# Kernel tuning notes

Hardware: AMD Instinct MI355X
Metric: run time of the kernel (lower is better)

## Reference

```python
import jax, jax.numpy as jnp
import numpy as np

H = 512   # layer_size
D = 5     # dim
B = 64
T = 512
EPS = 1e-3  # Keras BatchNormalization default epsilon


def _p(key, shape, scale=0.05):
    return jax.random.normal(key, shape, dtype=jnp.float32) * scale


def setup_inputs() -> dict:
    key = jax.random.key(0)
    ks = jax.random.split(key, 32)
    inp = {
        "x": jax.random.normal(ks[0], (B, T, D), dtype=jnp.float32),
        # LSTM 1 (input D)
        "W1": _p(ks[1], (D, 4 * H)), "U1": _p(ks[2], (H, 4 * H)), "b1": jnp.zeros((4 * H,), jnp.float32),
        # BatchNorm on H features (inference: moving stats)
        "g1": jnp.ones((H,), jnp.float32), "be1": jnp.zeros((H,), jnp.float32),
        "m1": _p(ks[3], (H,), 0.1), "v1": jnp.ones((H,), jnp.float32) + jax.random.uniform(ks[4], (H,)) * 0.1,
        # LSTM 2 (input H)
        "W2": _p(ks[5], (H, 4 * H)), "U2": _p(ks[6], (H, 4 * H)), "b2": jnp.zeros((4 * H,), jnp.float32),
        # LSTM 3 (input H, returns last state only)
        "W3": _p(ks[7], (H, 4 * H)), "U3": _p(ks[8], (H, 4 * H)), "b3": jnp.zeros((4 * H,), jnp.float32),
        # dense head y
        "d1w": _p(ks[9], (H, 32)), "d1b": jnp.zeros((32,), jnp.float32),
        "g2": jnp.ones((32,), jnp.float32), "be2": jnp.zeros((32,), jnp.float32),
        "m2": _p(ks[10], (32,), 0.1), "v2": jnp.ones((32,), jnp.float32) + jax.random.uniform(ks[11], (32,)) * 0.1,
        "d2w": _p(ks[12], (32, 16)), "d2b": jnp.zeros((16,), jnp.float32),
        "hw": _p(ks[13], (16, 1)), "hb": jnp.zeros((1,), jnp.float32),
        # dense head z
        "d4w": _p(ks[14], (H, 128)), "d4b": jnp.zeros((128,), jnp.float32),
        "d5w": _p(ks[15], (128, 64)), "d5b": jnp.zeros((64,), jnp.float32),
        "rw": _p(ks[16], (64, D)), "rb": jnp.zeros((D,), jnp.float32),
    }
    return inp


def lstm(x, W, U, b):
    """Keras LSTM, gate order i,f,c,o. x: [B,T,din] -> (seq [B,T,H], h_T, c_T)."""
    xz = jnp.einsum('btd,dk->btk', x, W) + b  # precompute input projections [B,T,4H]

    def step(carry, xz_t):
        h, c = carry
        z = xz_t + h @ U
        i, f, g, o = jnp.split(z, 4, axis=-1)
        i = jax.nn.sigmoid(i)
        f = jax.nn.sigmoid(f)
        g = jnp.tanh(g)
        o = jax.nn.sigmoid(o)
        c = f * c + i * g
        h = o * jnp.tanh(c)
        return (h, c), h

    b_ = x.shape[0]
    h0 = jnp.zeros((b_, U.shape[0]), x.dtype)
    (hT, cT), hs = jax.lax.scan(step, (h0, h0), jnp.swapaxes(xz, 0, 1))
    return jnp.swapaxes(hs, 0, 1), hT, cT


def bn_inf(x, g, b, m, v):
    return (x - m) * (g / jnp.sqrt(v + EPS)) + b


def reference(x, W1, U1, b1, g1, be1, m1, v1, W2, U2, b2, W3, U3, b3,
              d1w, d1b, g2, be2, m2, v2, d2w, d2b, hw, hb,
              d4w, d4b, d5w, d5b, rw, rb):
    # inference: GaussianNoise / Dropout are identity
    x1, h1, s1 = lstm(x, W1, U1, b1)          # [B,T,H]
    xr = bn_inf(x1, g1, be1, m1, v1)
    x2, h2, s2 = lstm(xr, W2, U2, b2)         # [B,T,H]
    xs = x1 + x2                               # residual Add
    _, h3, s3 = lstm(xs, W3, U3, b3)           # last hidden state [B,H]
    xlast = h3
    # head y
    y = xlast @ d1w + d1b
    y = bn_inf(y, g2, be2, m2, v2)
    y = y @ d2w + d2b
    y = jax.nn.sigmoid(y @ hw + hb)            # [B,1]
    # head z
    z = xlast @ d4w + d4b
    z = z @ d5w + d5b
    z = z @ rw + rb                            # [B,D]
    return (y, z)
```

## Files before the change

kernel.cpp:

```cpp
#include <hip/hip_runtime.h>
#include <hip/hip_bf16.h>

typedef short bf16x8 __attribute__((ext_vector_type(8)));
typedef float f32x4 __attribute__((ext_vector_type(4)));
typedef unsigned short u16;
typedef unsigned int u32;
typedef unsigned long long u64;

#define EPSBN 1e-3f

__device__ __forceinline__ u16 f2b(float f){
  unsigned u = __float_as_uint(f);
  return (u16)((u + 0x7fffu + ((u >> 16) & 1u)) >> 16);
}
__device__ __forceinline__ float b2f(u16 v){ return __uint_as_float(((unsigned)v) << 16); }
__device__ __forceinline__ float sigm(float x){ return 1.f/(1.f + __expf(-x)); }
__device__ __forceinline__ float tanhx(float x){ return 2.f/(1.f + __expf(-2.f*x)) - 1.f; }

union U64x2 { u64 q[2]; bf16x8 v; };
union BP    { u32 p[4]; bf16x8 v; };


__global__ void prep_sv(const float* __restrict__ g1, const float* __restrict__ be1,
                        const float* __restrict__ m1, const float* __restrict__ v1,
                        float* __restrict__ s, float* __restrict__ tv){
  int k = blockIdx.x*256 + threadIdx.x;
  if (k < 512){
    float sv = g1[k] * rsqrtf(v1[k] + EPSBN);
    s[k] = sv;
    tv[k] = be1[k] - m1[k]*sv;
  }
}

__global__ void prep_b2p(const float* __restrict__ W2, const float* __restrict__ b2,
                         const float* __restrict__ tv, float* __restrict__ out){
  int col = blockIdx.x*256 + threadIdx.x;
  float acc = b2[col];
  for (int k=0;k<512;++k) acc += tv[k] * W2[(size_t)k*2048 + col];
  out[col] = acc;
}

__global__ void transpose_pack(const float* __restrict__ in, const float* __restrict__ scale,
                               u16* __restrict__ out){
  __shared__ float tile[64][65];
  int k0 = blockIdx.x * 64;
  int c0 = blockIdx.y * 64;
  int t = threadIdx.x;
  int cc = t & 63, kk0 = (t >> 6) * 16;
  #pragma unroll
  for (int i=0;i<16;++i){
    float v = in[(size_t)(k0 + kk0 + i)*2048 + c0 + cc];
    if (scale) v *= scale[k0 + kk0 + i];
    tile[kk0 + i][cc] = v;
  }
  __syncthreads();
  int cc2 = t >> 2, kp = t & 3;
  int col = c0 + cc2;
  int hcol = col & 511;
  int row = (hcol >> 5)*128 + (col >> 9)*32 + ((hcol >> 4) & 1)*16 + (col & 15);
  bf16x8 v0, v1;
  #pragma unroll
  for (int i=0;i<8;++i){
    v0[i] = (short)f2b(tile[kp*16 + i][cc2]);
    v1[i] = (short)f2b(tile[kp*16 + 8 + i][cc2]);
  }
  u16* dst = out + (size_t)row*512 + k0 + kp*16;
  *(bf16x8*)dst = v0;
  *(bf16x8*)(dst + 8) = v1;
}

__global__ void pack_w1(const float* __restrict__ W1, u16* __restrict__ out){
  int r = blockIdx.x*256 + threadIdx.x;
  int wg = r >> 7, q = (r >> 5) & 3, jt = (r >> 4) & 1, jj = r & 15;
  int col = q*512 + wg*32 + jt*16 + jj;
  #pragma unroll
  for (int k=0;k<32;++k)
    out[(size_t)r*32 + k] = (k < 5) ? f2b(W1[(size_t)k*2048 + col]) : (u16)0;
}

__global__ void pack_x(const float* __restrict__ x, u16* __restrict__ out){
  int i = blockIdx.x*256 + threadIdx.x;
  int k = i & 31;
  int bt = i >> 5;
  out[i] = (k < 5) ? f2b(x[(size_t)bt*5 + k]) : (u16)0;
}

__global__ void __launch_bounds__(256, 1) scan_all(
    const u16* __restrict__ Ure1, const u16* __restrict__ Ure2, const u16* __restrict__ Ure3,
    const u16* __restrict__ W1p,  const u16* __restrict__ W2p,  const u16* __restrict__ W3p,
    const u16* __restrict__ xpad,
    const float* __restrict__ b1, const float* __restrict__ b2p, const float* __restrict__ b3,
    u32* __restrict__ hbuf_all,
    u32* __restrict__ x1seq,
    u32* __restrict__ xsseq,
    float* __restrict__ h3out, u32* __restrict__ cnt)
{
  const int bid = blockIdx.x;
  const int phase = bid >> 6;
  const int b6 = bid & 63;
  const int g = b6 & 3, wg = b6 >> 2;
  const int tid = threadIdx.x;
  const int w = tid >> 6, l = tid & 63;
  const int lm = l & 15, lh = l >> 4;
  const int bg0 = g * 16;
  const int b_own = tid & 15, jl = tid >> 4;
  const int pb = tid >> 4, pj = tid & 15;

  const u16* Ure  = phase == 0 ? Ure1 : (phase == 1 ? Ure2 : Ure3);
  const u16* Wre  = phase == 0 ? W1p  : (phase == 1 ? W2p  : W3p);
  const float* bias = phase == 0 ? b1 : (phase == 1 ? b2p : b3);
  u32* hbuf32 = hbuf_all + (size_t)phase * 65536;
  u32* seqout = phase == 0 ? x1seq : (phase == 1 ? xsseq : nullptr);
  const u32* upseq = phase == 1 ? x1seq : (phase == 2 ? xsseq : nullptr);

  u32* cq  = cnt + (phase*4 + g)*64;
  const u32* upq = (phase > 0) ? cnt + ((phase-1)*4 + g)*64 : nullptr;

  bf16x8 aU[8][4];
  #pragma unroll
  for (int q=0;q<4;++q)
    #pragma unroll
    for (int jt=0;jt<2;++jt){
      const u16* up = Ure + (size_t)(wg*128 + q*32 + jt*16 + lm)*512 + w*128 + lh*8;
      #pragma unroll
      for (int ks=0;ks<4;++ks) aU[q*2+jt][ks] = *(const bf16x8*)(up + ks*32);
    }
  bf16x8 aW[8][4];
  if (phase == 0){
    #pragma unroll
    for (int q=0;q<4;++q)
      #pragma unroll
      for (int jt=0;jt<2;++jt)
        aW[q*2+jt][0] = *(const bf16x8*)(Wre + (size_t)(wg*128 + q*32 + jt*16 + lm)*32 + lh*8);
  } else {
    #pragma unroll
    for (int q=0;q<4;++q)
      #pragma unroll
      for (int jt=0;jt<2;++jt){
        const u16* wp = Wre + (size_t)(wg*128 + q*32 + jt*16 + lm)*512 + w*128 + lh*8;
        #pragma unroll
        for (int ks=0;ks<4;++ks) aW[q*2+jt][ks] = *(const bf16x8*)(wp + ks*32);
      }
  }

  float bias_g[4][2];
  #pragma unroll
  for (int q=0;q<4;++q){
    bias_g[q][0] = bias[q*512 + wg*32 + jl];
    bias_g[q][1] = bias[q*512 + wg*32 + jl + 16];
  }

  float cs0 = 0.f, cs1 = 0.f;

  __shared__ float zex[8][4][16][18];
  __shared__ u16 hsh[16][34];
  __shared__ u16 xsh[16][34];
  __shared__ u32 x1w[16][17];

  const u64 tagmask = 0x0000FFFF0000FFFFull;

  for (int t=0; t<512; ++t){
    f32x4 acc[8] = {};

    if (phase == 0){
      if (w == 0){
        bf16x8 bx = *(const bf16x8*)(xpad + ((size_t)(bg0+lm)*512 + t)*32 + lh*8);
        #pragma unroll
        for (int i=0;i<8;++i)
          acc[i] = __builtin_amdgcn_mfma_f32_16x16x32_bf16(aW[i][0], bx, acc[i], 0,0,0);
      }
    } else {
      if (tid == 0){
        const u32 target = (u32)(16*(t+1));
        while (__hip_atomic_load(upq, __ATOMIC_RELAXED, __HIP_MEMORY_SCOPE_AGENT) < target) {}
      }
      __syncthreads();
      if (phase == 1){
        u32 rv = __hip_atomic_load(upseq + ((size_t)(bg0+pb)*512 + t)*256 + wg*16 + pj,
                                   __ATOMIC_RELAXED, __HIP_MEMORY_SCOPE_AGENT);
        x1w[pb][pj] = rv;
      }
      const u64* xp = (const u64*)upseq + ((size_t)(bg0+lm)*512 + t)*128 + w*32 + lh*2;
      U64x2 xq[4];
      #pragma unroll
      for (int ks=0;ks<4;++ks){
        xq[ks].q[0] = __hip_atomic_load(xp + ks*8,     __ATOMIC_RELAXED, __HIP_MEMORY_SCOPE_AGENT);
        xq[ks].q[1] = __hip_atomic_load(xp + ks*8 + 1, __ATOMIC_RELAXED, __HIP_MEMORY_SCOPE_AGENT);
      }
      #pragma unroll
      for (int ks=0;ks<4;++ks){
        #pragma unroll
        for (int i=0;i<8;++i)
          acc[i] = __builtin_amdgcn_mfma_f32_16x16x32_bf16(aW[i][ks], xq[ks].v, acc[i], 0,0,0);
      }
    }

    if (t > 0){
      const int slot = (t+1) & 1;
      const u64* hp = (const u64*)hbuf32
                    + (size_t)(slot*64 + bg0 + lm)*256 + w*64 + lh*4;
      const u32 tg = (u32)t;
      const u64 want = (u64)tg | ((u64)tg << 32);
      u64 raw[16];
      bool ok;
      do {
        #pragma unroll
        for (int ks=0;ks<4;++ks)
          #pragma unroll
          for (int qq=0;qq<4;++qq)
            raw[ks*4+qq] = __hip_atomic_load(hp + ks*16 + qq,
                                             __ATOMIC_RELAXED, __HIP_MEMORY_SCOPE_AGENT);
        u64 bad = 0;
        #pragma unroll
        for (int i=0;i<16;++i) bad |= (raw[i] & tagmask) ^ want;
        ok = __all(bad == 0);
      } while (!ok);
      #pragma unroll
      for (int ks=0;ks<4;++ks){
        BP bp;
        #pragma unroll
        for (int qq=0;qq<4;++qq){
          u32 lo = (u32)raw[ks*4+qq];
          u32 hi = (u32)(raw[ks*4+qq] >> 32);
          bp.p[qq] = (lo >> 16) | (hi & 0xFFFF0000u);
        }
        #pragma unroll
        for (int i=0;i<8;++i)
          acc[i] = __builtin_amdgcn_mfma_f32_16x16x32_bf16(aU[i][ks], bp.v, acc[i], 0,0,0);
      }
    }

    #pragma unroll
    for (int i=0;i<8;++i){
      #pragma unroll
      for (int r=0;r<4;++r)
        zex[i][w][lh*4 + r][lm] = acc[i][r];
    }
    __syncthreads();

    float hv0, hv1;
    {
      float zv[4][2];
      #pragma unroll
      for (int q=0;q<4;++q){
        #pragma unroll
        for (int s2=0;s2<2;++s2)
          zv[q][s2] = zex[q*2+s2][0][jl][b_own] + zex[q*2+s2][1][jl][b_own]
                    + zex[q*2+s2][2][jl][b_own] + zex[q*2+s2][3][jl][b_own] + bias_g[q][s2];
      }
      float iv = sigm(zv[0][0]), fv = sigm(zv[1][0]), gv = tanhx(zv[2][0]), ov = sigm(zv[3][0]);
      cs0 = fv * cs0 + iv * gv;
      hv0 = ov * tanhx(cs0);
      iv = sigm(zv[0][1]); fv = sigm(zv[1][1]); gv = tanhx(zv[2][1]); ov = sigm(zv[3][1]);
      cs1 = fv * cs1 + iv * gv;
      hv1 = ov * tanhx(cs1);
    }

    hsh[b_own][jl]      = f2b(hv0);
    hsh[b_own][jl + 16] = f2b(hv1);
    if (phase == 1){
      u32 w0 = x1w[b_own][jl >> 1], w1 = x1w[b_own][8 + (jl >> 1)];
      float x1r0 = b2f((u16)((jl & 1) ? (w0 >> 16) : (w0 & 0xffffu)));
      float x1r1 = b2f((u16)((jl & 1) ? (w1 >> 16) : (w1 & 0xffffu)));
      xsh[b_own][jl]      = f2b(x1r0 + hv0);
      xsh[b_own][jl + 16] = f2b(x1r1 + hv1);
    }
    if (phase == 2 && t == 511){
      h3out[(size_t)(bg0+b_own)*512 + wg*32 + jl]      = hv0;
      h3out[(size_t)(bg0+b_own)*512 + wg*32 + jl + 16] = hv1;
    }
    __syncthreads();

    {
      const int pslot = t & 1;
      const u32 tagv = (u32)(t + 1);
      u32 w0 = ((u32)hsh[pb][2*pj]     << 16) | tagv;
      u32 w1 = ((u32)hsh[pb][2*pj + 1] << 16) | tagv;
      __hip_atomic_store((u64*)(hbuf32 + (size_t)(pslot*64 + bg0 + pb)*512 + wg*32) + pj,
                         (u64)w0 | ((u64)w1 << 32),
                         __ATOMIC_RELAXED, __HIP_MEMORY_SCOPE_AGENT);
    }

    if (phase < 2){
      u32 sv;
      if (phase == 0) sv = (u32)hsh[pb][2*pj] | ((u32)hsh[pb][2*pj+1] << 16);
      else            sv = (u32)xsh[pb][2*pj] | ((u32)xsh[pb][2*pj+1] << 16);
      __hip_atomic_store(seqout + ((size_t)(bg0+pb)*512 + t)*256 + wg*16 + pj, sv,
                         __ATOMIC_RELAXED, __HIP_MEMORY_SCOPE_AGENT);
      asm volatile("s_waitcnt vmcnt(0)" ::: "memory");
      __syncthreads();
      if (tid == 0)
        __hip_atomic_fetch_add(cq, 1u, __ATOMIC_RELAXED, __HIP_MEMORY_SCOPE_AGENT);
    }
  }
}

__global__ void __launch_bounds__(256) head_k(
    const float* __restrict__ h3,
    const float* __restrict__ d1w, const float* __restrict__ d1b,
    const float* __restrict__ g2, const float* __restrict__ be2,
    const float* __restrict__ m2, const float* __restrict__ v2,
    const float* __restrict__ d2w, const float* __restrict__ d2b,
    const float* __restrict__ hw, const float* __restrict__ hb,
    const float* __restrict__ d4w, const float* __restrict__ d4b,
    const float* __restrict__ d5w, const float* __restrict__ d5b,
    const float* __restrict__ rw, const float* __restrict__ rb,
    float* __restrict__ out)
{
  __shared__ float hl[512];
  __shared__ float a1[32], a2[16], c1[128], c2[64];
  int b = blockIdx.x, t = threadIdx.x;
  for (int i=t; i<512; i+=256) hl[i] = h3[(size_t)b*512 + i];
  __syncthreads();
  if (t < 32){
    float acc = d1b[t];
    for (int k=0;k<512;++k) acc += hl[k] * d1w[(size_t)k*32 + t];
    a1[t] = (acc - m2[t]) * (g2[t] * rsqrtf(v2[t] + EPSBN)) + be2[t];
  } else if (t >= 128){
    int i = t - 128;
    float acc = d4b[i];
    for (int k=0;k<512;++k) acc += hl[k] * d4w[(size_t)k*128 + i];
    c1[i] = acc;
  }
  __syncthreads();
  if (t < 16){
    float acc = d2b[t];
    for (int k=0;k<32;++k) acc += a1[k] * d2w[k*16 + t];
    a2[t] = acc;
  } else if (t >= 64 && t < 128){
    int i = t - 64;
    float acc = d5b[i];
    for (int k=0;k<128;++k) acc += c1[k] * d5w[k*64 + i];
    c2[i] = acc;
  }
  __syncthreads();
  if (t == 0){
    float acc = hb[0];
    for (int k=0;k<16;++k) acc += a2[k] * hw[k];
    out[b] = 1.f/(1.f + __expf(-acc));
  } else if (t >= 32 && t < 37){
    int i = t - 32;
    float acc = rb[i];
    for (int k=0;k<64;++k) acc += c2[k] * rw[k*5 + i];
    out[64 + b*5 + i] = acc;
  }
}

extern "C" void kernel_launch(void* const* d_in, const int* in_sizes, int n_in,
                              void* d_out, int out_size, void* d_ws, size_t ws_size,
                              hipStream_t stream)
{
  const float* x   = (const float*)d_in[0];
  const float* W1  = (const float*)d_in[1];
  const float* U1  = (const float*)d_in[2];
  const float* b1  = (const float*)d_in[3];
  const float* g1  = (const float*)d_in[4];
  const float* be1 = (const float*)d_in[5];
  const float* m1  = (const float*)d_in[6];
  const float* v1  = (const float*)d_in[7];
  const float* W2  = (const float*)d_in[8];
  const float* U2  = (const float*)d_in[9];
  const float* b2  = (const float*)d_in[10];
  const float* W3  = (const float*)d_in[11];
  const float* U3  = (const float*)d_in[12];
  const float* b3  = (const float*)d_in[13];
  const float* d1w = (const float*)d_in[14];
  const float* d1b = (const float*)d_in[15];
  const float* g2  = (const float*)d_in[16];
  const float* be2 = (const float*)d_in[17];
  const float* m2  = (const float*)d_in[18];
  const float* v2  = (const float*)d_in[19];
  const float* d2w = (const float*)d_in[20];
  const float* d2b = (const float*)d_in[21];
  const float* hw  = (const float*)d_in[22];
  const float* hb  = (const float*)d_in[23];
  const float* d4w = (const float*)d_in[24];
  const float* d4b = (const float*)d_in[25];
  const float* d5w = (const float*)d_in[26];
  const float* d5b = (const float*)d_in[27];
  const float* rw  = (const float*)d_in[28];
  const float* rb  = (const float*)d_in[29];

  char* ws = (char*)d_ws;
  constexpr size_t SZ_W   = 2048ull*512*2;
  constexpr size_t o_Ure1 = 0;
  constexpr size_t o_Ure2 = o_Ure1 + SZ_W;
  constexpr size_t o_Ure3 = o_Ure2 + SZ_W;
  constexpr size_t o_W2p  = o_Ure3 + SZ_W;
  constexpr size_t o_W3p  = o_W2p + SZ_W;
  constexpr size_t o_W1p  = o_W3p + SZ_W;
  constexpr size_t o_xpad = o_W1p + 2048ull*32*2;
  constexpr size_t o_b2p  = o_xpad + 64ull*512*32*2;
  constexpr size_t o_s    = o_b2p + 2048ull*4;
  constexpr size_t o_tv   = o_s + 512ull*4;
  constexpr size_t o_h3   = o_tv + 512ull*4;
  constexpr size_t o_h    = o_h3 + 64ull*512*4;
  constexpr size_t SZ_HP  = 2ull*64*512*4;
  constexpr size_t SZ_H   = 3*SZ_HP;
  constexpr size_t o_cnt  = o_h + SZ_H;
  constexpr size_t o_x1   = o_cnt + 4096;
  constexpr size_t o_xs   = o_x1 + 64ull*512*512*2;

  u16* Ure1 = (u16*)(ws + o_Ure1);
  u16* Ure2 = (u16*)(ws + o_Ure2);
  u16* Ure3 = (u16*)(ws + o_Ure3);
  u16* W2p  = (u16*)(ws + o_W2p);
  u16* W3p  = (u16*)(ws + o_W3p);
  u16* W1p  = (u16*)(ws + o_W1p);
  u16* xpad = (u16*)(ws + o_xpad);
  u32* x1p  = (u32*)(ws + o_x1);
  u32* xsp  = (u32*)(ws + o_xs);

  hipMemsetAsync(ws + o_h, 0, SZ_H + 4096, stream);

  prep_sv<<<dim3(2), dim3(256), 0, stream>>>(g1, be1, m1, v1, (float*)(ws+o_s), (float*)(ws+o_tv));
  transpose_pack<<<dim3(8,32), dim3(256), 0, stream>>>(U1, nullptr, Ure1);
  transpose_pack<<<dim3(8,32), dim3(256), 0, stream>>>(U2, nullptr, Ure2);
  transpose_pack<<<dim3(8,32), dim3(256), 0, stream>>>(U3, nullptr, Ure3);
  transpose_pack<<<dim3(8,32), dim3(256), 0, stream>>>(W3, nullptr, W3p);
  transpose_pack<<<dim3(8,32), dim3(256), 0, stream>>>(W2, (const float*)(ws+o_s), W2p);
  prep_b2p<<<dim3(8), dim3(256), 0, stream>>>(W2, b2, (const float*)(ws+o_tv), (float*)(ws+o_b2p));
  pack_w1<<<dim3(8), dim3(256), 0, stream>>>(W1, W1p);
  pack_x<<<dim3(4096), dim3(256), 0, stream>>>(x, xpad);

  scan_all<<<dim3(192), dim3(256), 0, stream>>>(
      Ure1, Ure2, Ure3, W1p, W2p, W3p, xpad,
      b1, (const float*)(ws+o_b2p), b3,
      (u32*)(ws+o_h), x1p, xsp,
      (float*)(ws+o_h3), (u32*)(ws+o_cnt));

  head_k<<<dim3(64), dim3(256), 0, stream>>>((const float*)(ws+o_h3),
      d1w, d1b, g2, be2, m2, v2, d2w, d2b, hw, hb, d4w, d4b, d5w, d5b, rw, rb,
      (float*)d_out);
}
```

Before: 2.892 ms.

## Prefetch next-step upstream inputs and remove shared-memory staging in LSTM scan

Each thread now owns a pair of adjacent hidden units per batch row, so the gate results go straight to the global h-buffer and sequence output without passing through hsh/xsh/x1w shared arrays. The third __syncthreads is dropped and a raw s_barrier is used. The upstream-layer activations and x for step t+1 are prefetched during step t, with a non-blocking poll on the producer counter. The counter increment is deferred to the next step's barrier, which removes the per-step vmcnt(0) drain. The cost is a looser memory ordering: the counter publish relies on the barrier and implicit ordering of the earlier stores rather than an explicit wait, which could expose stale reads.

```diff
diff --git a/kernel.cpp b/kernel.cpp
--- a/kernel.cpp
+++ b/kernel.cpp
@@ -83,6 +83,10 @@
   int k = i & 31;
   int bt = i >> 5;
   out[i] = (k < 5) ? f2b(x[(size_t)bt*5 + k]) : (u16)0;
+}
+
+__device__ __forceinline__ void pollge(const u32* p, u32 target){
+  while (__hip_atomic_load(p, __ATOMIC_RELAXED, __HIP_MEMORY_SCOPE_AGENT) < target) {}
 }
 
 __global__ void __launch_bounds__(256, 1) scan_all(
@@ -103,8 +107,8 @@
   const int w = tid >> 6, l = tid & 63;
   const int lm = l & 15, lh = l >> 4;
   const int bg0 = g * 16;
-  const int b_own = tid & 15, jl = tid >> 4;
-  const int pb = tid >> 4, pj = tid & 15;
+  const int jp = tid & 15, gb = tid >> 4;
+  const int ti0 = jp >> 3;
 
   const u16* Ure  = phase == 0 ? Ure1 : (phase == 1 ? Ure2 : Ure3);
   const u16* Wre  = phase == 0 ? W1p  : (phase == 1 ? W2p  : W3p);
@@ -126,12 +130,15 @@
       for (int ks=0;ks<4;++ks) aU[q*2+jt][ks] = *(const bf16x8*)(up + ks*32);
     }
   bf16x8 aW[8][4];
+  bf16x8 aW1[8];
   if (phase == 0){
-    #pragma unroll
-    for (int q=0;q<4;++q)
-      #pragma unroll
-      for (int jt=0;jt<2;++jt)
-        aW[q*2+jt][0] = *(const bf16x8*)(Wre + (size_t)(wg*128 + q*32 + jt*16 + lm)*32 + lh*8);
+    if (w == 0){
+      #pragma unroll
+      for (int q=0;q<4;++q)
+        #pragma unroll
+        for (int jt=0;jt<2;++jt)
+          aW1[q*2+jt] = *(const bf16x8*)(Wre + (size_t)(wg*128 + q*32 + jt*16 + lm)*32 + lh*8);
+    }
   } else {
     #pragma unroll
     for (int q=0;q<4;++q)
@@ -143,50 +150,52 @@
       }
   }
 
-  float bias_g[4][2];
+  float bias0[4], bias1[4];
   #pragma unroll
   for (int q=0;q<4;++q){
-    bias_g[q][0] = bias[q*512 + wg*32 + jl];
-    bias_g[q][1] = bias[q*512 + wg*32 + jl + 16];
+    bias0[q] = bias[q*512 + wg*32 + 2*jp];
+    bias1[q] = bias[q*512 + wg*32 + 2*jp + 1];
   }
 
   float cs0 = 0.f, cs1 = 0.f;
 
   __shared__ float zex[8][4][16][18];
-  __shared__ u16 hsh[16][34];
-  __shared__ u16 xsh[16][34];
-  __shared__ u32 x1w[16][17];
-
   const u64 tagmask = 0x0000FFFF0000FFFFull;
+
+  U64x2 xq[4];
+  bf16x8 bx;
+  u32 rv = 0;
+  if (phase == 0){
+    if (w == 0)
+      bx = *(const bf16x8*)(xpad + ((size_t)(bg0+lm)*512 + 0)*32 + lh*8);
+  } else {
+    pollge(upq, 16u);
+    const u64* xp = (const u64*)upseq + ((size_t)(bg0+lm)*512 + 0)*128 + w*32 + lh*2;
+    #pragma unroll
+    for (int ks=0;ks<4;++ks){
+      xq[ks].q[0] = __hip_atomic_load(xp + ks*8,     __ATOMIC_RELAXED, __HIP_MEMORY_SCOPE_AGENT);
+      xq[ks].q[1] = __hip_atomic_load(xp + ks*8 + 1, __ATOMIC_RELAXED, __HIP_MEMORY_SCOPE_AGENT);
+    }
+    if (phase == 1)
+      rv = __hip_atomic_load(upseq + ((size_t)(bg0+gb)*512 + 0)*256 + wg*16 + jp,
+                             __ATOMIC_RELAXED, __HIP_MEMORY_SCOPE_AGENT);
+  }
 
   for (int t=0; t<512; ++t){
     f32x4 acc[8] = {};
+    const u32 rvc = rv;
+
+    u32 upv = 0xffffffffu;
+    if (phase > 0 && t < 511)
+      upv = __hip_atomic_load(upq, __ATOMIC_RELAXED, __HIP_MEMORY_SCOPE_AGENT);
 
     if (phase == 0){
       if (w == 0){
-        bf16x8 bx = *(const bf16x8*)(xpad + ((size_t)(bg0+lm)*512 + t)*32 + lh*8);
         #pragma unroll
         for (int i=0;i<8;++i)
-          acc[i] = __builtin_amdgcn_mfma_f32_16x16x32_bf16(aW[i][0], bx, acc[i], 0,0,0);
+          acc[i] = __builtin_amdgcn_mfma_f32_16x16x32_bf16(aW1[i], bx, acc[i], 0,0,0);
       }
     } else {
-      if (tid == 0){
-        const u32 target = (u32)(16*(t+1));
-        while (__hip_atomic_load(upq, __ATOMIC_RELAXED, __HIP_MEMORY_SCOPE_AGENT) < target) {}
-      }
-      __syncthreads();
-      if (phase == 1){
-        u32 rv = __hip_atomic_load(upseq + ((size_t)(bg0+pb)*512 + t)*256 + wg*16 + pj,
-                                   __ATOMIC_RELAXED, __HIP_MEMORY_SCOPE_AGENT);
-        x1w[pb][pj] = rv;
-      }
-      const u64* xp = (const u64*)upseq + ((size_t)(bg0+lm)*512 + t)*128 + w*32 + lh*2;
-      U64x2 xq[4];
-      #pragma unroll
-      for (int ks=0;ks<4;++ks){
-        xq[ks].q[0] = __hip_atomic_load(xp + ks*8,     __ATOMIC_RELAXED, __HIP_MEMORY_SCOPE_AGENT);
-        xq[ks].q[1] = __hip_atomic_load(xp + ks*8 + 1, __ATOMIC_RELAXED, __HIP_MEMORY_SCOPE_AGENT);
-      }
       #pragma unroll
       for (int ks=0;ks<4;++ks){
         #pragma unroll
@@ -230,68 +239,84 @@
       }
     }
 
+    if (t < 511){
+      if (phase == 0){
+        if (w == 0)
+          bx = *(const bf16x8*)(xpad + ((size_t)(bg0+lm)*512 + (t+1))*32 + lh*8);
+      } else {
+        const u32 tgt = 16u*(u32)(t+2);
+        if (upv < tgt) pollge(upq, tgt);
+        const u64* xp = (const u64*)upseq + ((size_t)(bg0+lm)*512 + (t+1))*128 + w*32 + lh*2;
+        #pragma unroll
+        for (int ks=0;ks<4;++ks){
+          xq[ks].q[0] = __hip_atomic_load(xp + ks*8,     __ATOMIC_RELAXED, __HIP_MEMORY_SCOPE_AGENT);
+          xq[ks].q[1] = __hip_atomic_load(xp + ks*8 + 1, __ATOMIC_RELAXED, __HIP_MEMORY_SCOPE_AGENT);
+        }
+        if (phase == 1)
+          rv = __hip_atomic_load(upseq + ((size_t)(bg0+gb)*512 + (t+1))*256 + wg*16 + jp,
+                                 __ATOMIC_RELAXED, __HIP_MEMORY_SCOPE_AGENT);
+      }
+    }
+
     #pragma unroll
     for (int i=0;i<8;++i){
       #pragma unroll
       for (int r=0;r<4;++r)
         zex[i][w][lh*4 + r][lm] = acc[i][r];
     }
-    __syncthreads();
-
-    float hv0, hv1;
+    asm volatile("s_waitcnt lgkmcnt(0)\n\ts_barrier" ::: "memory");
+
+    if (tid == 0 && phase < 2 && t > 0)
+      __hip_atomic_fetch_add(cq, 1u, __ATOMIC_RELAXED, __HIP_MEMORY_SCOPE_AGENT);
+
     {
-      float zv[4][2];
+      const int r0 = (2*jp) & 15, r1 = r0 + 1;
+      float zv0[4], zv1[4];
       #pragma unroll
       for (int q=0;q<4;++q){
-        #pragma unroll
-        for (int s2=0;s2<2;++s2)
-          zv[q][s2] = zex[q*2+s2][0][jl][b_own] + zex[q*2+s2][1][jl][b_own]
-                    + zex[q*2+s2][2][jl][b_own] + zex[q*2+s2][3][jl][b_own] + bias_g[q][s2];
-      }
-      float iv = sigm(zv[0][0]), fv = sigm(zv[1][0]), gv = tanhx(zv[2][0]), ov = sigm(zv[3][0]);
+        const int ti = q*2 + ti0;
+        zv0[q] = zex[ti][0][r0][gb] + zex[ti][1][r0][gb]
+               + zex[ti][2][r0][gb] + zex[ti][3][r0][gb] + bias0[q];
+        zv1[q] = zex[ti][0][r1][gb] + zex[ti][1][r1][gb]
+               + zex[ti][2][r1][gb] + zex[ti][3][r1][gb] + bias1[q];
+      }
+      float iv = sigm(zv0[0]), fv = sigm(zv0[1]), gv = tanhx(zv0[2]), ov = sigm(zv0[3]);
       cs0 = fv * cs0 + iv * gv;
-      hv0 = ov * tanhx(cs0);
-      iv = sigm(zv[0][1]); fv = sigm(zv[1][1]); gv = tanhx(zv[2][1]); ov = sigm(zv[3][1]);
+      float hv0 = ov * tanhx(cs0);
+      iv = sigm(zv1[0]); fv = sigm(zv1[1]); gv = tanhx(zv1[2]); ov = sigm(zv1[3]);
       cs1 = fv * cs1 + iv * gv;
-      hv1 = ov * tanhx(cs1);
-    }
-
-    hsh[b_own][jl]      = f2b(hv0);
-    hsh[b_own][jl + 16] = f2b(hv1);
-    if (phase == 1){
-      u32 w0 = x1w[b_own][jl >> 1], w1 = x1w[b_own][8 + (jl >> 1)];
-      float x1r0 = b2f((u16)((jl & 1) ? (w0 >> 16) : (w0 & 0xffffu)));
-      float x1r1 = b2f((u16)((jl & 1) ? (w1 >> 16) : (w1 & 0xffffu)));
-      xsh[b_own][jl]      = f2b(x1r0 + hv0);
-      xsh[b_own][jl + 16] = f2b(x1r1 + hv1);
-    }
-    if (phase == 2 && t == 511){
-      h3out[(size_t)(bg0+b_own)*512 + wg*32 + jl]      = hv0;
-      h3out[(size_t)(bg0+b_own)*512 + wg*32 + jl + 16] = hv1;
-    }
-    __syncthreads();
-
-    {
-      const int pslot = t & 1;
+      float hv1 = ov * tanhx(cs1);
+
       const u32 tagv = (u32)(t + 1);
-      u32 w0 = ((u32)hsh[pb][2*pj]     << 16) | tagv;
-      u32 w1 = ((u32)hsh[pb][2*pj + 1] << 16) | tagv;
-      __hip_atomic_store((u64*)(hbuf32 + (size_t)(pslot*64 + bg0 + pb)*512 + wg*32) + pj,
+      u32 w0 = ((u32)f2b(hv0) << 16) | tagv;
+      u32 w1 = ((u32)f2b(hv1) << 16) | tagv;
+      __hip_atomic_store((u64*)(hbuf32 + (size_t)((t&1)*64 + bg0 + gb)*512 + wg*32) + jp,
                          (u64)w0 | ((u64)w1 << 32),
                          __ATOMIC_RELAXED, __HIP_MEMORY_SCOPE_AGENT);
-    }
-
-    if (phase < 2){
-      u32 sv;
-      if (phase == 0) sv = (u32)hsh[pb][2*pj] | ((u32)hsh[pb][2*pj+1] << 16);
-      else            sv = (u32)xsh[pb][2*pj] | ((u32)xsh[pb][2*pj+1] << 16);
-      __hip_atomic_store(seqout + ((size_t)(bg0+pb)*512 + t)*256 + wg*16 + pj, sv,
-                         __ATOMIC_RELAXED, __HIP_MEMORY_SCOPE_AGENT);
-      asm volatile("s_waitcnt vmcnt(0)" ::: "memory");
-      __syncthreads();
-      if (tid == 0)
-        __hip_atomic_fetch_add(cq, 1u, __ATOMIC_RELAXED, __HIP_MEMORY_SCOPE_AGENT);
-    }
+
+      if (phase == 0){
+        u32 sv = (u32)f2b(hv0) | ((u32)f2b(hv1) << 16);
+        __hip_atomic_store(seqout + ((size_t)(bg0+gb)*512 + t)*256 + wg*16 + jp, sv,
+                           __ATOMIC_RELAXED, __HIP_MEMORY_SCOPE_AGENT);
+      } else if (phase == 1){
+        float x1r0 = b2f((u16)(rvc & 0xffffu));
+        float x1r1 = b2f((u16)(rvc >> 16));
+        u32 sv = (u32)f2b(x1r0 + hv0) | ((u32)f2b(x1r1 + hv1) << 16);
+        __hip_atomic_store(seqout + ((size_t)(bg0+gb)*512 + t)*256 + wg*16 + jp, sv,
+                           __ATOMIC_RELAXED, __HIP_MEMORY_SCOPE_AGENT);
+      } else if (t == 511){
+        h3out[(size_t)(bg0+gb)*512 + wg*32 + 2*jp]     = hv0;
+        h3out[(size_t)(bg0+gb)*512 + wg*32 + 2*jp + 1] = hv1;
+      }
+    }
+    asm volatile("s_barrier" ::: "memory");
+  }
+
+  if (phase < 2){
+    asm volatile("s_waitcnt vmcnt(0)" ::: "memory");
+    __syncthreads();
+    if (tid == 0)
+      __hip_atomic_fetch_add(cq, 1u, __ATOMIC_RELAXED, __HIP_MEMORY_SCOPE_AGENT);
   }
 }
 
```

New measurement: 2.340 ms. 1.24x faster.
